# Optimization experiments

Hardware: AMD Instinct MI355X
Metric: run time of the kernel (lower is better)

## Reference

```python
import jax, jax.numpy as jnp
import numpy as np

N = 32768   # total nodes
B = 128     # graphs
S = 256     # nodes per graph (equal-size graphs)
E = 524288  # edges
DIN = 128   # in_dim
DH = 256    # hidden_dim
H = 8       # heads
DFF = 1024  # ffn hidden
EPS = 1e-5


def _seg_sum(x, idx, num):
    return jax.ops.segment_sum(x, idx, num_segments=num)


def _bn(x, g, b):
    # BatchNorm1d with batch statistics (training-mode math, deterministic)
    mu = jnp.mean(x, axis=0)
    var = jnp.mean((x - mu) ** 2, axis=0)
    return (x - mu) * jax.lax.rsqrt(var + EPS) * g + b


def _ln(x, g, b):
    mu = jnp.mean(x, axis=-1, keepdims=True)
    var = jnp.mean((x - mu) ** 2, axis=-1, keepdims=True)
    return (x - mu) * jax.lax.rsqrt(var + EPS) * g + b


def _gcn_conv(x, W, bias, edge_index, n):
    # PyG GCNConv: h = x W; add self-loops; norm = d^-1/2[row] * d^-1/2[col]; scatter-add at col
    h = x @ W
    loop = jnp.arange(n)
    row = jnp.concatenate([edge_index[0], loop])
    col = jnp.concatenate([edge_index[1], loop])
    deg = _seg_sum(jnp.ones_like(col, dtype=h.dtype), col, n)  # >=1 due to self-loops
    dis = jax.lax.rsqrt(jnp.maximum(deg, 1.0))
    norm = dis[row] * dis[col]
    out = _seg_sum(h[row] * norm[:, None], col, n)
    return out + bias


def setup_inputs() -> dict:
    key = jax.random.key(0)
    ks = jax.random.split(key, 24)

    def w(i, shape, scale=0.05):
        return jax.random.normal(ks[i], shape, dtype=jnp.float32) * scale

    return {
        "x": jax.random.normal(ks[0], (N, DIN), dtype=jnp.float32),
        "edge_index": jax.random.randint(ks[1], (2, E), 0, N, dtype=jnp.int32),
        "batch": jnp.repeat(jnp.arange(B, dtype=jnp.int32), S),
        "inter_f": jax.random.normal(ks[2], (B, DH), dtype=jnp.float32),
        "bn1_g": jnp.ones((DIN,), jnp.float32), "bn1_b": jnp.zeros((DIN,), jnp.float32),
        "bn2_g": jnp.ones((DH,), jnp.float32), "bn2_b": jnp.zeros((DH,), jnp.float32),
        "w_conv1": w(3, (DIN, DH)), "b_conv1": jnp.zeros((DH,), jnp.float32),
        "w_conv2": w(4, (DH, DH)), "b_conv2": jnp.zeros((DH,), jnp.float32),
        "wq": w(5, (DH, DH)), "bq": jnp.zeros((DH,), jnp.float32),
        "wk": w(6, (DH, DH)), "bk": jnp.zeros((DH,), jnp.float32),
        "wv": w(7, (DH, DH)), "bv": jnp.zeros((DH,), jnp.float32),
        "wo": w(8, (DH, DH)), "bo": jnp.zeros((DH,), jnp.float32),
        "ln1_g": jnp.ones((DH,), jnp.float32), "ln1_b": jnp.zeros((DH,), jnp.float32),
        "ln2_g": jnp.ones((DH,), jnp.float32), "ln2_b": jnp.zeros((DH,), jnp.float32),
        "w_ff1": w(9, (DH, DFF)), "b_ff1": jnp.zeros((DFF,), jnp.float32),
        "w_ff2": w(10, (DFF, DH)), "b_ff2": jnp.zeros((DH,), jnp.float32),
    }


def reference(x, edge_index, batch, inter_f,
              bn1_g, bn1_b, bn2_g, bn2_b,
              w_conv1, b_conv1, w_conv2, b_conv2,
              wq, bq, wk, bk, wv, bv, wo, bo,
              ln1_g, ln1_b, ln2_g, ln2_b,
              w_ff1, b_ff1, w_ff2, b_ff2):
    n = x.shape[0]
    hd = DH // H
    # init_avg_h: scatter-mean of raw x per graph
    cnt = _seg_sum(jnp.ones((n,), x.dtype), batch, B)
    init_avg_h = _seg_sum(x, batch, B) / jnp.maximum(cnt, 1.0)[:, None]
    # layer 1 (dropout = identity in eval)
    h = _bn(x, bn1_g, bn1_b)
    h = jax.nn.relu(_gcn_conv(h, w_conv1, b_conv1, edge_index, n))
    # layer 2 with residual
    pre = h
    h2 = _bn(h, bn2_g, bn2_b)
    h = pre + jax.nn.relu(_gcn_conv(h2, w_conv2, b_conv2, edge_index, n))
    # transformer block: inject per-graph feature, self-attend within each graph
    inter_h = inter_f[batch]
    t = (h + inter_h).reshape(B, S, DH)
    q = (t @ wq + bq).reshape(B, S, H, hd)
    k = (t @ wk + bk).reshape(B, S, H, hd)
    v = (t @ wv + bv).reshape(B, S, H, hd)
    scores = jnp.einsum('bqhd,bkhd->bhqk', q, k) / jnp.sqrt(jnp.float32(hd))
    attn = jax.nn.softmax(scores, axis=-1)
    o = jnp.einsum('bhqk,bkhd->bqhd', attn, v).reshape(B, S, DH) @ wo + bo
    t2 = _ln(t + o, ln1_g, ln1_b)
    ffn = jax.nn.relu(t2 @ w_ff1 + b_ff1) @ w_ff2 + b_ff2
    t3 = _ln(t2 + ffn, ln2_g, ln2_b)
    hg = t3.reshape(n, DH)
    readout = _seg_sum(hg, batch, B)
    return readout, init_avg_h
```

## Files before the change

### kernel.cpp

```cpp
#include <hip/hip_runtime.h>
#include <math.h>

#define NN   32768
#define BG   128
#define SG   256
#define EE   524288
#define DIN_ 128
#define DH_  256
#define NH   8
#define HD_  32
#define DFF_ 1024
#define EPS_ 1e-5f

typedef __attribute__((ext_vector_type(8))) short bf16x8;
typedef __attribute__((ext_vector_type(4))) float f32x4;
typedef __attribute__((ext_vector_type(2))) unsigned int u32x2;
typedef __attribute__((ext_vector_type(4))) unsigned int u32x4;

__device__ __forceinline__ unsigned short f2bf(float f) {
    unsigned int u = __builtin_bit_cast(unsigned int, f);
    unsigned int r = u + 0x7FFFu + ((u >> 16) & 1u);
    return (unsigned short)(r >> 16);
}
__device__ __forceinline__ float bf2f(unsigned short u) {
    return __builtin_bit_cast(float, (unsigned int)u << 16);
}
__device__ __forceinline__ unsigned int pack2bf(float a, float b) {
    return (unsigned int)f2bf(a) | ((unsigned int)f2bf(b) << 16);
}
__device__ __forceinline__ void glds16(const unsigned short* g, unsigned short* l) {
    __builtin_amdgcn_global_load_lds(
        (const __attribute__((address_space(1))) void*)g,
        (__attribute__((address_space(3))) void*)l, 16, 0, 0);
}
#define WAIT_VM4() __builtin_amdgcn_s_waitcnt(0x0F74)
#define WAIT_VM2() __builtin_amdgcn_s_waitcnt(0x0F72)
#define WAIT_VM1() __builtin_amdgcn_s_waitcnt(0x0F71)
#define WAIT_VM0() __builtin_amdgcn_s_waitcnt(0x0F70)

#define QSCALE (0.17677669529663689f * 1.4426950408889634f)

__global__ __launch_bounds__(128) void initavg_kernel(const float* __restrict__ X,
                                                      float* __restrict__ out2) {
    int b = blockIdx.x, j = threadIdx.x;
    float s = 0.f;
    for (int r = 0; r < SG; ++r) s += X[(size_t)(b * SG + r) * DIN_ + j];
    out2[b * DIN_ + j] = s * (1.f / (float)SG);
}

template <int C>
__global__ __launch_bounds__(C) void colstats_kernel(const float* __restrict__ X,
                                                     float* __restrict__ csum,
                                                     float* __restrict__ csumsq) {
    int j = threadIdx.x;
    size_t r0 = (size_t)blockIdx.x * 256;
    float s = 0.f, sq = 0.f;
    for (int r = 0; r < 256; ++r) {
        float v = X[(r0 + r) * C + j];
        s += v; sq += v * v;
    }
    atomicAdd(&csum[j], s);
    atomicAdd(&csumsq[j], sq);
}

template <int C>
__global__ __launch_bounds__(C) void colstats_b_kernel(const unsigned short* __restrict__ X,
                                                       float* __restrict__ csum,
                                                       float* __restrict__ csumsq) {
    int j = threadIdx.x;
    size_t r0 = (size_t)blockIdx.x * 256;
    float s = 0.f, sq = 0.f;
    for (int r = 0; r < 256; ++r) {
        float v = bf2f(X[(r0 + r) * C + j]);
        s += v; sq += v * v;
    }
    atomicAdd(&csum[j], s);
    atomicAdd(&csumsq[j], sq);
}

template <int C>
__global__ __launch_bounds__(C) void bnfin_kernel(const float* __restrict__ csum,
                                                  const float* __restrict__ csumsq,
                                                  const float* __restrict__ g,
                                                  const float* __restrict__ b,
                                                  float* __restrict__ scale,
                                                  float* __restrict__ shift) {
    int j = threadIdx.x;
    float mu  = csum[j] * (1.f / (float)NN);
    float var = csumsq[j] * (1.f / (float)NN) - mu * mu;
    float s = g[j] * rsqrtf(var + EPS_);
    scale[j] = s;
    shift[j] = b[j] - mu * s;
}

template <int C>
__global__ __launch_bounds__(256) void bnapply_kernel(const float* __restrict__ X,
                                                      const float* __restrict__ sc,
                                                      const float* __restrict__ sh,
                                                      unsigned short* __restrict__ Y) {
    int i = blockIdx.x * 256 + threadIdx.x;
    int j = i & (C - 1);
    Y[i] = f2bf(X[i] * sc[j] + sh[j]);
}

__global__ __launch_bounds__(256) void wtrans_kernel(const float* __restrict__ W,
                                                     unsigned short* __restrict__ Wt,
                                                     int K, int N, float scale) {
    int idx = blockIdx.x * 256 + threadIdx.x;
    if (idx < K * N) {
        int n = idx / K, k = idx - n * K;
        Wt[idx] = f2bf(W[(size_t)k * N + n] * scale);
    }
}

__global__ __launch_bounds__(256) void bcat_kernel(const float* __restrict__ bq,
                                                   const float* __restrict__ bk,
                                                   const float* __restrict__ bv,
                                                   float* __restrict__ o) {
    int j = threadIdx.x;
    if (blockIdx.x == 0) o[j] = bq[j] * QSCALE;
    else if (blockIdx.x == 1) o[DH_ + j] = bk[j];
    else o[2 * DH_ + j] = bv[j];
}

__global__ __launch_bounds__(256) void deg_kernel(const int* __restrict__ col,
                                                  int* __restrict__ deg) {
    int e = blockIdx.x * 256 + threadIdx.x;
    if (e < EE) atomicAdd(&deg[col[e]], 1);
}

__global__ __launch_bounds__(1024) void scan_kernel(const int* __restrict__ deg,
                                                    int* __restrict__ off,
                                                    float* __restrict__ dis) {
    __shared__ int sums[1024];
    int t = threadIdx.x;
    int base = t * 32;
    int loc[32];
    int run = 0;
#pragma unroll
    for (int i = 0; i < 32; ++i) { loc[i] = run; run += deg[base + i]; }
    sums[t] = run;
    __syncthreads();
    for (int d = 1; d < 1024; d <<= 1) {
        int tmp = (t >= d) ? sums[t - d] : 0;
        __syncthreads();
        sums[t] += tmp;
        __syncthreads();
    }
    int excl = sums[t] - run;
#pragma unroll
    for (int i = 0; i < 32; ++i) {
        off[base + i] = excl + loc[i];
        dis[base + i] = rsqrtf((float)(deg[base + i] + 1));
    }
    if (t == 1023) off[NN] = sums[1023];
}

__global__ __launch_bounds__(256) void scatter_kernel(const int* __restrict__ row,
                                                      const int* __restrict__ col,
                                                      const int* __restrict__ off,
                                                      int* __restrict__ cnt,
                                                      int* __restrict__ srow) {
    int e = blockIdx.x * 256 + threadIdx.x;
    if (e < EE) {
        int c = col[e];
        int p = off[c] + atomicAdd(&cnt[c], 1);
        srow[p] = row[e];
    }
}

template <int C, int FUSE_BN>
__global__ __launch_bounds__(256) void aggb_kernel(const unsigned short* __restrict__ X,
                                                   const int* __restrict__ off,
                                                   const int* __restrict__ srow,
                                                   const float* __restrict__ dis,
                                                   const float* __restrict__ scl,
                                                   const float* __restrict__ shf,
                                                   unsigned short* __restrict__ Y) {
    constexpr int EPL = C / 64;
    int lane = threadIdx.x & 63;
    int c = blockIdx.x * 4 + (threadIdx.x >> 6);
    float dc = dis[c];
    float acc[EPL];
    float wsum = dc;
    {
        unsigned short t[EPL];
        const unsigned short* xc = X + (size_t)c * C + lane * EPL;
        if constexpr (EPL == 4) *(uint2*)t = *(const uint2*)xc;
        else *(unsigned int*)t = *(const unsigned int*)xc;
#pragma unroll
        for (int e2 = 0; e2 < EPL; ++e2) acc[e2] = dc * bf2f(t[e2]);
    }
    int s = off[c], en = off[c + 1];
    int i = s;
    for (; i + 4 <= en; i += 4) {
        int r0 = srow[i], r1 = srow[i + 1], r2 = srow[i + 2], r3 = srow[i + 3];
        float d0 = dis[r0], d1 = dis[r1], d2 = dis[r2], d3 = dis[r3];
        unsigned short t0[EPL], t1[EPL], t2[EPL], t3[EPL];
        const unsigned short* p0 = X + (size_t)r0 * C + lane * EPL;
        const unsigned short* p1 = X + (size_t)r1 * C + lane * EPL;
        const unsigned short* p2 = X + (size_t)r2 * C + lane * EPL;
        const unsigned short* p3 = X + (size_t)r3 * C + lane * EPL;
        if constexpr (EPL == 4) {
            *(uint2*)t0 = *(const uint2*)p0;
            *(uint2*)t1 = *(const uint2*)p1;
            *(uint2*)t2 = *(const uint2*)p2;
            *(uint2*)t3 = *(const uint2*)p3;
        } else {
            *(unsigned int*)t0 = *(const unsigned int*)p0;
            *(unsigned int*)t1 = *(const unsigned int*)p1;
            *(unsigned int*)t2 = *(const unsigned int*)p2;
            *(unsigned int*)t3 = *(const unsigned int*)p3;
        }
        wsum += d0 + d1 + d2 + d3;
#pragma unroll
        for (int e2 = 0; e2 < EPL; ++e2) {
            acc[e2] += d0 * bf2f(t0[e2]) + d1 * bf2f(t1[e2]) +
                       d2 * bf2f(t2[e2]) + d3 * bf2f(t3[e2]);
        }
    }
    for (; i < en; ++i) {
        int r = srow[i];
        float dr = dis[r];
        unsigned short t[EPL];
        const unsigned short* xr = X + (size_t)r * C + lane * EPL;
        if constexpr (EPL == 4) *(uint2*)t = *(const uint2*)xr;
        else *(unsigned int*)t = *(const unsigned int*)xr;
        wsum += dr;
#pragma unroll
        for (int e2 = 0; e2 < EPL; ++e2) acc[e2] += dr * bf2f(t[e2]);
    }
    unsigned short t[EPL];
#pragma unroll
    for (int e2 = 0; e2 < EPL; ++e2) {
        float v;
        if constexpr (FUSE_BN) {
            int j = lane * EPL + e2;
            v = dc * (scl[j] * acc[e2] + shf[j] * wsum);
        } else {
            v = dc * acc[e2];
        }
        t[e2] = f2bf(v);
    }
    unsigned short* yc = Y + (size_t)c * C + lane * EPL;
    if constexpr (EPL == 4) *(uint2*)yc = *(const uint2*)t;
    else *(unsigned int*)yc = *(const unsigned int*)t;
}

template <int MT>
__global__ __launch_bounds__(512, 8) void gemm_bf16_kernel(
    const unsigned short* __restrict__ A,
    const unsigned short* __restrict__ Bt,
    unsigned short* __restrict__ Cb,
    int M, int K, int N,
    const float* __restrict__ bias,
    const unsigned short* __restrict__ resb,
    const float* __restrict__ inter,
    int do_relu, int relu_first) {
    constexpr int LDP = 32;
    constexpr int CP = 136;
    constexpr int MI = MT / 64;
    constexpr int STG = (MT == 128) ? 8192 : 6144;
    constexpr int BOFS = (MT == 128) ? 4096 : 2048;
    constexpr int SMEMSZ = 3 * STG;
    __shared__ unsigned short Smem[SMEMSZ];
    unsigned short* Cs = Smem;
    int gx = gridDim.x, gyP = gridDim.y >> 3;
    int d = blockIdx.y * gx + blockIdx.x;
    int xcd = d & 7, j2 = d >> 3;
    int bm = (xcd * gyP + j2 / gx) * MT;
    int bn = (j2 % gx) * 128;
    int tid = threadIdx.x;
    int wave = tid >> 6, lane = tid & 63;
    int wm = (wave >> 1) * (MT / 4);
    int wn = (wave & 1) * 64;
    int lrc = lane & 15;
    int koct = lane >> 4;
    int rsw = (lrc >> 1) & 3;
    int rofs = (koct ^ rsw) * 8;

    int cg = (lane & 3) ^ ((lane >> 3) & 3);
    int skk = cg * 8;

    const unsigned short* g0 = nullptr;
    int lofs64 = 0;
    int nloads = 2;
    size_t gstride16 = 0;
    if constexpr (MT == 64) {
        if (wave < 4) {
            int sr = wave * 32 + (lane >> 2);
            g0 = Bt + (size_t)(bn + sr) * K + skk;
            lofs64 = BOFS + wave * 1024 + lane * 8;
            nloads = 2;
            gstride16 = (size_t)16 * K;
        } else {
            int sr = (wave - 4) * 16 + (lane >> 2);
            g0 = A + (size_t)(bm + sr) * K + skk;
            lofs64 = (wave - 4) * 512 + lane * 8;
            nloads = 1;
        }
    }
    const unsigned short* gA0 = nullptr;
    const unsigned short* gB0 = nullptr;
    int lofs = 0;
    if constexpr (MT == 128) {
        int sr = wave * 16 + (lane >> 2);
        gA0 = A + (size_t)(bm + sr) * K + skk;
        gB0 = Bt + (size_t)(bn + sr) * K + skk;
        lofs = wave * 512 + lane * 8;
    }

    f32x4 acc[MI][4];
#pragma unroll
    for (int i = 0; i < MI; ++i)
#pragma unroll
        for (int j = 0; j < 4; ++j) acc[i][j] = (f32x4){0.f, 0.f, 0.f, 0.f};

    if constexpr (MT == 128) {
        glds16(gA0, Smem + lofs);
        glds16(gB0, Smem + BOFS + lofs);
        glds16(gA0 + 32, Smem + STG + lofs);
        glds16(gB0 + 32, Smem + STG + BOFS + lofs);
    } else {
        glds16(g0, Smem + lofs64);
        if (nloads == 2) glds16(g0 + gstride16, Smem + lofs64 + 512);
        glds16(g0 + 32, Smem + STG + lofs64);
        if (nloads == 2) glds16(g0 + 32 + gstride16, Smem + STG + lofs64 + 512);
    }

    int rb = 0;
    for (int k0 = 0; k0 < K; k0 += 32) {
        if (k0 + 64 < K) {
            int wb = rb + 2; if (wb >= 3) wb -= 3;
            unsigned short* ld = Smem + wb * STG;
            if constexpr (MT == 128) {
                glds16(gA0 + k0 + 64, ld + lofs);
                glds16(gB0 + k0 + 64, ld + BOFS + lofs);
                WAIT_VM4();
            } else {
                glds16(g0 + k0 + 64, ld + lofs64);
                if (nloads == 2) {
                    glds16(g0 + k0 + 64 + gstride16, ld + lofs64 + 512);
                    WAIT_VM4();
                } else {
                    WAIT_VM2();
                }
            }
        } else if (k0 + 32 < K) {
            if constexpr (MT == 128) WAIT_VM2();
            else { if (nloads == 2) WAIT_VM2(); else WAIT_VM1(); }
        } else {
            WAIT_VM0();
        }
        __builtin_amdgcn_s_barrier();
        const unsigned short* Ab = Smem + rb * STG;
        const unsigned short* Bb = Ab + BOFS;
        bf16x8 af[MI], bfr[4];
#pragma unroll
        for (int i = 0; i < MI; ++i)
            af[i] = *(const bf16x8*)(Ab + (wm + i * 16 + lrc) * LDP + rofs);
#pragma unroll
        for (int j = 0; j < 4; ++j)
            bfr[j] = *(const bf16x8*)(Bb + (wn + j * 16 + lrc) * LDP + rofs);
#pragma unroll
        for (int i = 0; i < MI; ++i)
#pragma unroll
            for (int j = 0; j < 4; ++j)
                acc[i][j] = __builtin_amdgcn_mfma_f32_16x16x32_bf16(af[i], bfr[j],
                                                                    acc[i][j], 0, 0, 0);
        __builtin_amdgcn_s_barrier();
        rb = (rb + 1 == 3) ? 0 : rb + 1;
    }
#pragma unroll
    for (int i = 0; i < MI; ++i) {
#pragma unroll
        for (int r = 0; r < 4; ++r) {
            int lrow = wm + i * 16 + koct * 4 + r;
            int grow = bm + lrow;
#pragma unroll
            for (int j = 0; j < 4; ++j) {
                int lcol = wn + j * 16 + lrc;
                int gcol = bn + lcol;
                float v = acc[i][j][r];
                if (bias) v += bias[gcol];
                if (relu_first) v = fmaxf(v, 0.f);
                if (resb) v += bf2f(resb[(size_t)grow * N + gcol]);
                if (inter) v += inter[(grow >> 8) * N + gcol];
                if (do_relu && !relu_first) v = fmaxf(v, 0.f);
                Cs[lrow * CP + lcol] = f2bf(v);
            }
        }
    }
    __syncthreads();
#pragma unroll
    for (int it = 0; it < MT / 32; ++it) {
        int row = it * 32 + (tid >> 4);
        int cc = (tid & 15) * 8;
        *(uint4*)(&Cb[(size_t)(bm + row) * N + bn + cc]) =
            *(const uint4*)(&Cs[row * CP + cc]);
    }
}

__global__ __launch_bounds__(256, 4) void attn_mfma_kernel(
    const unsigned short* __restrict__ QKV,
    unsigned short* __restrict__ Ob) {
    int b = blockIdx.x >> 3, h = blockIdx.x & 7;
    __shared__ unsigned short Ks[256 * 32];
    __shared__ unsigned short Vt[32 * 264];
    __shared__ float Lc[4 * 64];
    const unsigned short* kg = QKV + (size_t)b * 256 * 768 + 256 + h * 32;
    const unsigned short* vg = QKV + (size_t)b * 256 * 768 + 512 + h * 32;
    int tid = threadIdx.x;
#pragma unroll
    for (int it = 0; it < 4; ++it) {
        int c = it * 256 + tid;
        int row = c >> 2, ch = c & 3;
        int slot = ch ^ ((row >> 1) & 3);
        *(uint4*)(Ks + row * 32 + slot * 8) =
            *(const uint4*)(kg + (size_t)row * 768 + ch * 8);
    }
#pragma unroll
    for (int it = 0; it < 4; ++it) {
        int c = it * 256 + tid;
        int key = c >> 2, d0 = (c & 3) * 8;
        unsigned short tmp[8];
        *(uint4*)tmp = *(const uint4*)(vg + (size_t)key * 768 + d0);
#pragma unroll
        for (int j = 0; j < 8; ++j) Vt[(d0 + j) * 264 + key] = tmp[j];
    }
    __syncthreads();

    int wave = tid >> 6, lane = tid & 63;
    int lr = lane & 15, koct = lane >> 4;
    int s4 = (lr >> 1) & 3;
    int qrow0 = b * 256 + wave * 64;
    bf16x8 qf[4];
#pragma unroll
    for (int j = 0; j < 4; ++j)
        qf[j] = *(const bf16x8*)(QKV + (size_t)(qrow0 + j * 16 + lr) * 768 + h * 32 + koct * 8);

    f32x4 Oa[4][2];
    float lp[4];
#pragma unroll
    for (int i = 0; i < 4; ++i) {
        Oa[i][0] = (f32x4){0.f, 0.f, 0.f, 0.f};
        Oa[i][1] = (f32x4){0.f, 0.f, 0.f, 0.f};
        lp[i] = 0.f;
    }
    float* Lw = Lc + wave * 64;

    for (int kc = 0; kc < 256; kc += 32) {
        bf16x8 kf0 = *(const bf16x8*)(Ks + (kc + lr) * 32 + (koct ^ s4) * 8);
        bf16x8 kf1 = *(const bf16x8*)(Ks + (kc + 16 + lr) * 32 + (koct ^ s4) * 8);
        bf16x8 pfr[4];
#pragma unroll
        for (int j = 0; j < 4; ++j) {
            f32x4 St0 = __builtin_amdgcn_mfma_f32_16x16x32_bf16(kf0, qf[j],
                            (f32x4){0.f, 0.f, 0.f, 0.f}, 0, 0, 0);
            f32x4 St1 = __builtin_amdgcn_mfma_f32_16x16x32_bf16(kf1, qf[j],
                            (f32x4){0.f, 0.f, 0.f, 0.f}, 0, 0, 0);
            float p0[4], p1[4], ps = 0.f;
#pragma unroll
            for (int r = 0; r < 4; ++r) {
                p0[r] = exp2f(St0[r]); p1[r] = exp2f(St1[r]);
                ps += p0[r] + p1[r];
            }
            lp[j] += ps;
            unsigned int w0a, w0b, w1a, w1b;
            asm("v_cvt_pk_bf16_f32 %0, %1, %2" : "=v"(w0a) : "v"(p0[0]), "v"(p0[1]));
            asm("v_cvt_pk_bf16_f32 %0, %1, %2" : "=v"(w0b) : "v"(p0[2]), "v"(p0[3]));
            asm("v_cvt_pk_bf16_f32 %0, %1, %2" : "=v"(w1a) : "v"(p1[0]), "v"(p1[1]));
            asm("v_cvt_pk_bf16_f32 %0, %1, %2" : "=v"(w1b) : "v"(p1[2]), "v"(p1[3]));
            u32x2 sa = __builtin_amdgcn_permlane32_swap(w0a, w1a, false, false);
            u32x2 da = __builtin_amdgcn_permlane16_swap(sa[0], sa[1], false, false);
            u32x2 sb = __builtin_amdgcn_permlane32_swap(w0b, w1b, false, false);
            u32x2 db = __builtin_amdgcn_permlane16_swap(sb[0], sb[1], false, false);
            u32x4 pw = {da[0], db[0], da[1], db[1]};
            pfr[j] = __builtin_bit_cast(bf16x8, pw);
        }
        bf16x8 vf0 = *(const bf16x8*)(Vt + lr * 264 + kc + koct * 8);
        bf16x8 vf1 = *(const bf16x8*)(Vt + (16 + lr) * 264 + kc + koct * 8);
#pragma unroll
        for (int i = 0; i < 4; ++i) {
            Oa[i][0] = __builtin_amdgcn_mfma_f32_16x16x32_bf16(pfr[i], vf0, Oa[i][0], 0, 0, 0);
            Oa[i][1] = __builtin_amdgcn_mfma_f32_16x16x32_bf16(pfr[i], vf1, Oa[i][1], 0, 0, 0);
        }
    }
#pragma unroll
    for (int j = 0; j < 4; ++j) {
        lp[j] += __shfl_xor(lp[j], 16);
        lp[j] += __shfl_xor(lp[j], 32);
    }
    if (koct == 0) {
#pragma unroll
        for (int j = 0; j < 4; ++j) Lw[j * 16 + lr] = lp[j];
    }
    __builtin_amdgcn_s_waitcnt(0);
#pragma unroll
    for (int i = 0; i < 4; ++i) {
        f32x4 l4 = *(const f32x4*)(Lw + i * 16 + koct * 4);
#pragma unroll
        for (int r = 0; r < 4; ++r) {
            float inv = 1.f / l4[r];
            int row = qrow0 + i * 16 + koct * 4 + r;
#pragma unroll
            for (int jn = 0; jn < 2; ++jn) {
                int col = h * 32 + jn * 16 + lr;
                Ob[(size_t)row * 256 + col] = f2bf(Oa[i][jn][r] * inv);
            }
        }
    }
}

__global__ __launch_bounds__(256) void lnb_kernel(const unsigned short* __restrict__ Z,
                                                  unsigned short* __restrict__ Out,
                                                  const float* __restrict__ g,
                                                  const float* __restrict__ bt) {
    int row = blockIdx.x * 4 + (threadIdx.x >> 6);
    int lane = threadIdx.x & 63;
    unsigned short tv[4];
    *(uint2*)tv = *(const uint2*)(Z + (size_t)row * DH_ + lane * 4);
    float v[4];
    float sum = 0.f;
#pragma unroll
    for (int i = 0; i < 4; ++i) { v[i] = bf2f(tv[i]); sum += v[i]; }
#pragma unroll
    for (int off = 32; off; off >>= 1) sum += __shfl_xor(sum, off);
    float mu = sum * (1.f / (float)DH_);
    float vs = 0.f;
#pragma unroll
    for (int i = 0; i < 4; ++i) { float dd = v[i] - mu; vs += dd * dd; }
#pragma unroll
    for (int off = 32; off; off >>= 1) vs += __shfl_xor(vs, off);
    float rs = rsqrtf(vs * (1.f / (float)DH_) + EPS_);
    float4 gv = *(const float4*)(g + lane * 4);
    float4 bv = *(const float4*)(bt + lane * 4);
    unsigned short ov[4];
    ov[0] = f2bf((v[0] - mu) * rs * gv.x + bv.x);
    ov[1] = f2bf((v[1] - mu) * rs * gv.y + bv.y);
    ov[2] = f2bf((v[2] - mu) * rs * gv.z + bv.z);
    ov[3] = f2bf((v[3] - mu) * rs * gv.w + bv.w);
    *(uint2*)(Out + (size_t)row * DH_ + lane * 4) = *(uint2*)ov;
}

__global__ __launch_bounds__(256) void readout_kernel(const unsigned short* __restrict__ T3,
                                                      float* __restrict__ out) {
    int b = blockIdx.x, j = threadIdx.x;
    float s = 0.f;
    for (int r = 0; r < SG; ++r) s += bf2f(T3[(size_t)(b * SG + r) * DH_ + j]);
    out[b * DH_ + j] = s;
}

extern "C" void kernel_launch(void* const* d_in, const int* in_sizes, int n_in,
                              void* d_out, int out_size, void* d_ws, size_t ws_size,
                              hipStream_t stream) {
    const float* x       = (const float*)d_in[0];
    const int*   ei      = (const int*)d_in[1];
    const float* inter_f = (const float*)d_in[3];
    const float* bn1_g = (const float*)d_in[4],  *bn1_b = (const float*)d_in[5];
    const float* bn2_g = (const float*)d_in[6],  *bn2_b = (const float*)d_in[7];
    const float* w_conv1 = (const float*)d_in[8],  *b_conv1 = (const float*)d_in[9];
    const float* w_conv2 = (const float*)d_in[10], *b_conv2 = (const float*)d_in[11];
    const float* wq = (const float*)d_in[12], *bq = (const float*)d_in[13];
    const float* wk = (const float*)d_in[14], *bk = (const float*)d_in[15];
    const float* wv = (const float*)d_in[16], *bv = (const float*)d_in[17];
    const float* wo = (const float*)d_in[18], *bo = (const float*)d_in[19];
    const float* ln1_g = (const float*)d_in[20], *ln1_b = (const float*)d_in[21];
    const float* ln2_g = (const float*)d_in[22], *ln2_b = (const float*)d_in[23];
    const float* w_ff1 = (const float*)d_in[24], *b_ff1 = (const float*)d_in[25];
    const float* w_ff2 = (const float*)d_in[26], *b_ff2 = (const float*)d_in[27];
    float* out = (float*)d_out;

    char* base = (char*)d_ws;
    size_t o = 0;
    auto alloc = [&](size_t bytes) -> void* {
        void* p = base + o;
        o = (o + bytes + 255) & ~(size_t)255;
        return p;
    };
    int*   deg    = (int*)alloc(NN * 4);
    int*   off    = (int*)alloc((NN + 1) * 4);
    int*   cnt    = (int*)alloc(NN * 4);
    int*   srow   = (int*)alloc(EE * 4);
    float* dis    = (float*)alloc(NN * 4);
    float* csum   = (float*)alloc(256 * 4);
    float* csumsq = (float*)alloc(256 * 4);
    float* scl    = (float*)alloc(256 * 4);
    float* shf    = (float*)alloc(256 * 4);
    float* bqkv   = (float*)alloc(768 * 4);
    const size_t SLOT = (size_t)NN * DH_;
    unsigned short* Arena = (unsigned short*)alloc((size_t)NN * DFF_ * 2);
    unsigned short* TB = (unsigned short*)alloc(SLOT * 2);
    unsigned short* B0 = (unsigned short*)alloc(SLOT * 2);
    unsigned short* wc1t  = (unsigned short*)alloc((size_t)DIN_ * DH_ * 2);
    unsigned short* wc2t  = (unsigned short*)alloc((size_t)DH_ * DH_ * 2);
    unsigned short* wqkvt = (unsigned short*)alloc((size_t)DH_ * DH_ * 3 * 2);
    unsigned short* wot   = (unsigned short*)alloc((size_t)DH_ * DH_ * 2);
    unsigned short* wf1t  = (unsigned short*)alloc((size_t)DH_ * DFF_ * 2);
    unsigned short* wf2t  = (unsigned short*)alloc((size_t)DFF_ * DH_ * 2);
    unsigned short* Xa   = Arena;
    unsigned short* X2a  = Arena + (size_t)NN * DIN_;
    unsigned short* QKVb = Arena;
    unsigned short* zb   = Arena + SLOT * 3;
    unsigned short* Fb   = Arena;
    unsigned short* tb   = TB;
    unsigned short* z2b  = TB;

    hipMemsetAsync(deg, 0, NN * 4, stream);
    hipMemsetAsync(cnt, 0, NN * 4, stream);
    hipMemsetAsync(csum, 0, 2048, stream);

    wtrans_kernel<<<(DIN_ * DH_ + 255) / 256, 256, 0, stream>>>(w_conv1, wc1t, DIN_, DH_, 1.f);
    wtrans_kernel<<<(DH_ * DH_ + 255) / 256, 256, 0, stream>>>(w_conv2, wc2t, DH_, DH_, 1.f);
    wtrans_kernel<<<(DH_ * DH_ + 255) / 256, 256, 0, stream>>>(wq, wqkvt, DH_, DH_, QSCALE);
    wtrans_kernel<<<(DH_ * DH_ + 255) / 256, 256, 0, stream>>>(wk, wqkvt + DH_ * DH_, DH_, DH_, 1.f);
    wtrans_kernel<<<(DH_ * DH_ + 255) / 256, 256, 0, stream>>>(wv, wqkvt + 2 * DH_ * DH_, DH_, DH_, 1.f);
    wtrans_kernel<<<(DH_ * DH_ + 255) / 256, 256, 0, stream>>>(wo, wot, DH_, DH_, 1.f);
    wtrans_kernel<<<(DH_ * DFF_ + 255) / 256, 256, 0, stream>>>(w_ff1, wf1t, DH_, DFF_, 1.f);
    wtrans_kernel<<<(DFF_ * DH_ + 255) / 256, 256, 0, stream>>>(w_ff2, wf2t, DFF_, DH_, 1.f);
    bcat_kernel<<<3, 256, 0, stream>>>(bq, bk, bv, bqkv);

    initavg_kernel<<<BG, 128, 0, stream>>>(x, out + BG * DH_);

    colstats_kernel<DIN_><<<NN / 256, DIN_, 0, stream>>>(x, csum, csumsq);
    bnfin_kernel<DIN_><<<1, DIN_, 0, stream>>>(csum, csumsq, bn1_g, bn1_b, scl, shf);
    bnapply_kernel<DIN_><<<NN * DIN_ / 256, 256, 0, stream>>>(x, scl, shf, B0);

    deg_kernel<<<EE / 256, 256, 0, stream>>>(ei + EE, deg);
    scan_kernel<<<1, 1024, 0, stream>>>(deg, off, dis);
    scatter_kernel<<<EE / 256, 256, 0, stream>>>(ei, ei + EE, off, cnt, srow);

    aggb_kernel<DIN_, 0><<<NN / 4, 256, 0, stream>>>(B0, off, srow, dis,
                                                     nullptr, nullptr, Xa);
    gemm_bf16_kernel<64><<<dim3(DH_ / 128, NN / 64), 512, 0, stream>>>(
        Xa, wc1t, B0, NN, DIN_, DH_, b_conv1, nullptr, nullptr, 1, 0);

    hipMemsetAsync(csum, 0, 2048, stream);
    colstats_b_kernel<DH_><<<NN / 256, DH_, 0, stream>>>(B0, csum, csumsq);
    bnfin_kernel<DH_><<<1, DH_, 0, stream>>>(csum, csumsq, bn2_g, bn2_b, scl, shf);

    aggb_kernel<DH_, 1><<<NN / 4, 256, 0, stream>>>(B0, off, srow, dis,
                                                    scl, shf, X2a);
    gemm_bf16_kernel<64><<<dim3(DH_ / 128, NN / 64), 512, 0, stream>>>(
        X2a, wc2t, tb, NN, DH_, DH_, b_conv2, B0, inter_f, 1, 1);

    gemm_bf16_kernel<128><<<dim3(768 / 128, NN / 128), 512, 0, stream>>>(
        tb, wqkvt, QKVb, NN, DH_, 768, bqkv, nullptr, nullptr, 0, 0);

    attn_mfma_kernel<<<BG * NH, 256, 0, stream>>>(QKVb, B0);

    gemm_bf16_kernel<64><<<dim3(DH_ / 128, NN / 64), 512, 0, stream>>>(
        B0, wot, zb, NN, DH_, DH_, bo, tb, nullptr, 0, 0);
    lnb_kernel<<<NN / 4, 256, 0, stream>>>(zb, B0, ln1_g, ln1_b);

    gemm_bf16_kernel<128><<<dim3(DFF_ / 128, NN / 128), 512, 0, stream>>>(
        B0, wf1t, Fb, NN, DH_, DFF_, b_ff1, nullptr, nullptr, 1, 0);
    gemm_bf16_kernel<64><<<dim3(DH_ / 128, NN / 64), 512, 0, stream>>>(
        Fb, wf2t, z2b, NN, DFF_, DH_, b_ff2, B0, nullptr, 0, 0);

    lnb_kernel<<<NN / 4, 256, 0, stream>>>(z2b, B0, ln2_g, ln2_b);
    readout_kernel<<<BG, 256, 0, stream>>>(B0, out);
}
```

Measured before the change: 540.9 us.

## Add 64-row GEMM kernel loading B fragments directly into registers

Adds a new gemm64_kernel, templated on K, for the N=256 GEMMs (conv1, conv2, out-proj, FFN2). In it only the A tile is staged through LDS, and each wave loads its weight (B) fragments straight from global memory into registers with a one-step software prefetch. The step loop is fully unrolled with hand-tuned vmcnt waits. The aim is to cut LDS traffic and footprint, which may raise occupancy, at the cost of redundant weight reads from cache and more registers. The old 128-row GEMM is de-templated and kept for the QKV and FFN1 GEMMs.

```diff
diff --git a/kernel.cpp b/kernel.cpp
--- a/kernel.cpp
+++ b/kernel.cpp
@@ -33,10 +33,14 @@
         (const __attribute__((address_space(1))) void*)g,
         (__attribute__((address_space(3))) void*)l, 16, 0, 0);
 }
-#define WAIT_VM4() __builtin_amdgcn_s_waitcnt(0x0F74)
-#define WAIT_VM2() __builtin_amdgcn_s_waitcnt(0x0F72)
-#define WAIT_VM1() __builtin_amdgcn_s_waitcnt(0x0F71)
-#define WAIT_VM0() __builtin_amdgcn_s_waitcnt(0x0F70)
+#define WAIT_VM0()  __builtin_amdgcn_s_waitcnt(0x0F70)
+#define WAIT_VM1()  __builtin_amdgcn_s_waitcnt(0x0F71)
+#define WAIT_VM2()  __builtin_amdgcn_s_waitcnt(0x0F72)
+#define WAIT_VM4()  __builtin_amdgcn_s_waitcnt(0x0F74)
+#define WAIT_VM8()  __builtin_amdgcn_s_waitcnt(0x0F78)
+#define WAIT_VM10() __builtin_amdgcn_s_waitcnt(0x0F7A)
+#define WAIT_VM13() __builtin_amdgcn_s_waitcnt(0x0F7D)
+#define WAIT_VM14() __builtin_amdgcn_s_waitcnt(0x0F7E)
 
 #define QSCALE (0.17677669529663689f * 1.4426950408889634f)
 
@@ -247,7 +251,6 @@
     else *(unsigned int*)yc = *(const unsigned int*)t;
 }
 
-template <int MT>
 __global__ __launch_bounds__(512, 8) void gemm_bf16_kernel(
     const unsigned short* __restrict__ A,
     const unsigned short* __restrict__ Bt,
@@ -259,20 +262,20 @@
     int do_relu, int relu_first) {
     constexpr int LDP = 32;
     constexpr int CP = 136;
-    constexpr int MI = MT / 64;
-    constexpr int STG = (MT == 128) ? 8192 : 6144;
-    constexpr int BOFS = (MT == 128) ? 4096 : 2048;
+    constexpr int MI = 2;
+    constexpr int STG = 8192;
+    constexpr int BOFS = 4096;
     constexpr int SMEMSZ = 3 * STG;
     __shared__ unsigned short Smem[SMEMSZ];
     unsigned short* Cs = Smem;
     int gx = gridDim.x, gyP = gridDim.y >> 3;
     int d = blockIdx.y * gx + blockIdx.x;
     int xcd = d & 7, j2 = d >> 3;
-    int bm = (xcd * gyP + j2 / gx) * MT;
+    int bm = (xcd * gyP + j2 / gx) * 128;
     int bn = (j2 % gx) * 128;
     int tid = threadIdx.x;
     int wave = tid >> 6, lane = tid & 63;
-    int wm = (wave >> 1) * (MT / 4);
+    int wm = (wave >> 1) * 32;
     int wn = (wave & 1) * 64;
     int lrc = lane & 15;
     int koct = lane >> 4;
@@ -282,33 +285,10 @@
     int cg = (lane & 3) ^ ((lane >> 3) & 3);
     int skk = cg * 8;
 
-    const unsigned short* g0 = nullptr;
-    int lofs64 = 0;
-    int nloads = 2;
-    size_t gstride16 = 0;
-    if constexpr (MT == 64) {
-        if (wave < 4) {
-            int sr = wave * 32 + (lane >> 2);
-            g0 = Bt + (size_t)(bn + sr) * K + skk;
-            lofs64 = BOFS + wave * 1024 + lane * 8;
-            nloads = 2;
-            gstride16 = (size_t)16 * K;
-        } else {
-            int sr = (wave - 4) * 16 + (lane >> 2);
-            g0 = A + (size_t)(bm + sr) * K + skk;
-            lofs64 = (wave - 4) * 512 + lane * 8;
-            nloads = 1;
-        }
-    }
-    const unsigned short* gA0 = nullptr;
-    const unsigned short* gB0 = nullptr;
-    int lofs = 0;
-    if constexpr (MT == 128) {
-        int sr = wave * 16 + (lane >> 2);
-        gA0 = A + (size_t)(bm + sr) * K + skk;
-        gB0 = Bt + (size_t)(bn + sr) * K + skk;
-        lofs = wave * 512 + lane * 8;
-    }
+    int sr = wave * 16 + (lane >> 2);
+    const unsigned short* gA0 = A + (size_t)(bm + sr) * K + skk;
+    const unsigned short* gB0 = Bt + (size_t)(bn + sr) * K + skk;
+    int lofs = wave * 512 + lane * 8;
 
     f32x4 acc[MI][4];
 #pragma unroll
@@ -316,39 +296,21 @@
 #pragma unroll
         for (int j = 0; j < 4; ++j) acc[i][j] = (f32x4){0.f, 0.f, 0.f, 0.f};
 
-    if constexpr (MT == 128) {
-        glds16(gA0, Smem + lofs);
-        glds16(gB0, Smem + BOFS + lofs);
-        glds16(gA0 + 32, Smem + STG + lofs);
-        glds16(gB0 + 32, Smem + STG + BOFS + lofs);
-    } else {
-        glds16(g0, Smem + lofs64);
-        if (nloads == 2) glds16(g0 + gstride16, Smem + lofs64 + 512);
-        glds16(g0 + 32, Smem + STG + lofs64);
-        if (nloads == 2) glds16(g0 + 32 + gstride16, Smem + STG + lofs64 + 512);
-    }
+    glds16(gA0, Smem + lofs);
+    glds16(gB0, Smem + BOFS + lofs);
+    glds16(gA0 + 32, Smem + STG + lofs);
+    glds16(gB0 + 32, Smem + STG + BOFS + lofs);
 
     int rb = 0;
     for (int k0 = 0; k0 < K; k0 += 32) {
         if (k0 + 64 < K) {
             int wb = rb + 2; if (wb >= 3) wb -= 3;
             unsigned short* ld = Smem + wb * STG;
-            if constexpr (MT == 128) {
-                glds16(gA0 + k0 + 64, ld + lofs);
-                glds16(gB0 + k0 + 64, ld + BOFS + lofs);
-                WAIT_VM4();
-            } else {
-                glds16(g0 + k0 + 64, ld + lofs64);
-                if (nloads == 2) {
-                    glds16(g0 + k0 + 64 + gstride16, ld + lofs64 + 512);
-                    WAIT_VM4();
-                } else {
-                    WAIT_VM2();
-                }
-            }
+            glds16(gA0 + k0 + 64, ld + lofs);
+            glds16(gB0 + k0 + 64, ld + BOFS + lofs);
+            WAIT_VM4();
         } else if (k0 + 32 < K) {
-            if constexpr (MT == 128) WAIT_VM2();
-            else { if (nloads == 2) WAIT_VM2(); else WAIT_VM1(); }
+            WAIT_VM2();
         } else {
             WAIT_VM0();
         }
@@ -393,7 +355,109 @@
     }
     __syncthreads();
 #pragma unroll
-    for (int it = 0; it < MT / 32; ++it) {
+    for (int it = 0; it < 4; ++it) {
+        int row = it * 32 + (tid >> 4);
+        int cc = (tid & 15) * 8;
+        *(uint4*)(&Cb[(size_t)(bm + row) * N + bn + cc]) =
+            *(const uint4*)(&Cs[row * CP + cc]);
+    }
+}
+
+template <int KC>
+__global__ __launch_bounds__(512, 8) void gemm64_kernel(
+    const unsigned short* __restrict__ A,
+    const unsigned short* __restrict__ Bt,
+    unsigned short* __restrict__ Cb,
+    int N,
+    const float* __restrict__ bias,
+    const unsigned short* __restrict__ resb,
+    const float* __restrict__ inter,
+    int do_relu, int relu_first) {
+    constexpr int NSTEP = KC / 32;
+    constexpr int CP = 136;
+    constexpr int STG = 2048;
+    constexpr int SMEMSZ = 64 * CP;
+    __shared__ unsigned short Smem[SMEMSZ];
+    unsigned short* Cs = Smem;
+    int gx = gridDim.x, gyP = gridDim.y >> 3;
+    int d = blockIdx.y * gx + blockIdx.x;
+    int xcd = d & 7, j2 = d >> 3;
+    int bm = (xcd * gyP + j2 / gx) * 64;
+    int bn = (j2 % gx) * 128;
+    int tid = threadIdx.x;
+    int wave = tid >> 6, lane = tid & 63;
+    int wm = (wave >> 1) * 16;
+    int wn = (wave & 1) * 64;
+    int lrc = lane & 15;
+    int koct = lane >> 4;
+    int rsw = (lrc >> 1) & 3;
+    int rofs = (koct ^ rsw) * 8;
+    int cg = (lane & 3) ^ ((lane >> 3) & 3);
+    int skk = cg * 8;
+
+    const unsigned short* g0 = A + (size_t)(bm + wave * 16 + (lane >> 2)) * KC + skk;
+    unsigned short* l0 = Smem + wave * 512 + lane * 8;
+    const unsigned short* gB = Bt + (size_t)(bn + wn + lrc) * KC + koct * 8;
+
+    f32x4 acc[4];
+#pragma unroll
+    for (int j = 0; j < 4; ++j) acc[j] = (f32x4){0.f, 0.f, 0.f, 0.f};
+
+    if (wave < 4) {
+        glds16(g0, l0);
+        glds16(g0 + 32, l0 + STG);
+    }
+    bf16x8 bcur[4], bnxt[4];
+#pragma unroll
+    for (int j = 0; j < 4; ++j)
+        bcur[j] = *(const bf16x8*)(gB + (size_t)j * 16 * KC);
+
+#pragma unroll
+    for (int t = 0; t < NSTEP; ++t) {
+        int k0 = t * 32;
+        if (t + 2 < NSTEP && wave < 4)
+            glds16(g0 + k0 + 64, Smem + ((t + 2) % 3) * STG + wave * 512 + lane * 8);
+        if (t + 1 < NSTEP) {
+#pragma unroll
+            for (int j = 0; j < 4; ++j)
+                bnxt[j] = *(const bf16x8*)(gB + (size_t)j * 16 * KC + k0 + 32);
+        }
+        if (wave < 4) {
+            if (t == 0) WAIT_VM10();
+            else if (t == NSTEP - 1) WAIT_VM8();
+            else if (t == NSTEP - 2) WAIT_VM13();
+            else WAIT_VM14();
+        }
+        __builtin_amdgcn_s_barrier();
+        const unsigned short* Ab = Smem + (t % 3) * STG;
+        bf16x8 af = *(const bf16x8*)(Ab + (wm + lrc) * 32 + rofs);
+#pragma unroll
+        for (int j = 0; j < 4; ++j)
+            acc[j] = __builtin_amdgcn_mfma_f32_16x16x32_bf16(af, bcur[j], acc[j], 0, 0, 0);
+        __builtin_amdgcn_s_barrier();
+#pragma unroll
+        for (int j = 0; j < 4; ++j) bcur[j] = bnxt[j];
+    }
+#pragma unroll
+    for (int r = 0; r < 4; ++r) {
+        int lrow = wm + koct * 4 + r;
+        int grow = bm + lrow;
+#pragma unroll
+        for (int j = 0; j < 4; ++j) {
+            int lcol = wn + j * 16 + lrc;
+            int gcol = bn + lcol;
+            float v = acc[j][r];
+            if (bias) v += bias[gcol];
+            if (relu_first) v = fmaxf(v, 0.f);
+            if (resb) v += bf2f(resb[(size_t)grow * N + gcol]);
+            if (inter) v += inter[(grow >> 8) * N + gcol];
+            if (do_relu && !relu_first) v = fmaxf(v, 0.f);
+            Cs[lrow * CP + lcol] = f2bf(v);
+        }
+    }
+    __syncthreads();
+#pragma unroll
+    for (int it = 0; it < 2; ++it) {
         int row = it * 32 + (tid >> 4);
         int cc = (tid & 15) * 8;
         *(uint4*)(&Cb[(size_t)(bm + row) * N + bn + cc]) =
@@ -632,8 +696,8 @@
 
     aggb_kernel<DIN_, 0><<<NN / 4, 256, 0, stream>>>(B0, off, srow, dis,
                                                      nullptr, nullptr, Xa);
-    gemm_bf16_kernel<64><<<dim3(DH_ / 128, NN / 64), 512, 0, stream>>>(
-        Xa, wc1t, B0, NN, DIN_, DH_, b_conv1, nullptr, nullptr, 1, 0);
+    gemm64_kernel<128><<<dim3(DH_ / 128, NN / 64), 512, 0, stream>>>(
+        Xa, wc1t, B0, DH_, b_conv1, nullptr, nullptr, 1, 0);
 
     hipMemsetAsync(csum, 0, 2048, stream);
     colstats_b_kernel<DH_><<<NN / 256, DH_, 0, stream>>>(B0, csum, csumsq);
@@ -641,22 +705,22 @@
 
     aggb_kernel<DH_, 1><<<NN / 4, 256, 0, stream>>>(B0, off, srow, dis,
                                                     scl, shf, X2a);
-    gemm_bf16_kernel<64><<<dim3(DH_ / 128, NN / 64), 512, 0, stream>>>(
-        X2a, wc2t, tb, NN, DH_, DH_, b_conv2, B0, inter_f, 1, 1);
-
-    gemm_bf16_kernel<128><<<dim3(768 / 128, NN / 128), 512, 0, stream>>>(
+    gemm64_kernel<256><<<dim3(DH_ / 128, NN / 64), 512, 0, stream>>>(
+        X2a, wc2t, tb, DH_, b_conv2, B0, inter_f, 1, 1);
+
+    gemm_bf16_kernel<<<dim3(768 / 128, NN / 128), 512, 0, stream>>>(
         tb, wqkvt, QKVb, NN, DH_, 768, bqkv, nullptr, nullptr, 0, 0);
 
     attn_mfma_kernel<<<BG * NH, 256, 0, stream>>>(QKVb, B0);
 
-    gemm_bf16_kernel<64><<<dim3(DH_ / 128, NN / 64), 512, 0, stream>>>(
-        B0, wot, zb, NN, DH_, DH_, bo, tb, nullptr, 0, 0);
+    gemm64_kernel<256><<<dim3(DH_ / 128, NN / 64), 512, 0, stream>>>(
+        B0, wot, zb, DH_, bo, tb, nullptr, 0, 0);
     lnb_kernel<<<NN / 4, 256, 0, stream>>>(zb, B0, ln1_g, ln1_b);
 
-    gemm_bf16_kernel<128><<<dim3(DFF_ / 128, NN / 128), 512, 0, stream>>>(
+    gemm_bf16_kernel<<<dim3(DFF_ / 128, NN / 128), 512, 0, stream>>>(
         B0, wf1t, Fb, NN, DH_, DFF_, b_ff1, nullptr, nullptr, 1, 0);
-    gemm_bf16_kernel<64><<<dim3(DH_ / 128, NN / 64), 512, 0, stream>>>(
-        Fb, wf2t, z2b, NN, DFF_, DH_, b_ff2, B0, nullptr, 0, 0);
+    gemm64_kernel<1024><<<dim3(DH_ / 128, NN / 64), 512, 0, stream>>>(
+        Fb, wf2t, z2b, DH_, b_ff2, B0, nullptr, 0, 0);
 
     lnb_kernel<<<NN / 4, 256, 0, stream>>>(z2b, B0, ln2_g, ln2_b);
     readout_kernel<<<BG, 256, 0, stream>>>(B0, out);
```

New measurement: 699.5 us. 29.3% more time.
